# Kernel optimization log

Hardware: AMD Instinct MI355X
Metric: run time of the kernel (lower is better)

## Reference

```python
import jax, jax.numpy as jnp
import numpy as np

B, D, H, W, C = 1, 16, 56, 56, 256
WD, WH, WW = 2, 7, 7
SD, SH, SW = 1, 3, 3
HEADS = 8
HDIM = C // HEADS
N = WD * WH * WW          # 98 tokens per window
NW = (D // WD) * (H // WH) * (W // WW)  # 512 windows per batch element
HID = 4 * C


def _rel_index():
    coords = np.stack(np.meshgrid(np.arange(WD), np.arange(WH), np.arange(WW), indexing='ij')).reshape(3, -1)
    rel = (coords[:, :, None] - coords[:, None, :]).transpose(1, 2, 0).astype(np.int64)
    rel[..., 0] += WD - 1; rel[..., 1] += WH - 1; rel[..., 2] += WW - 1
    rel[..., 0] *= (2 * WH - 1) * (2 * WW - 1)
    rel[..., 1] *= (2 * WW - 1)
    return rel.sum(-1)  # (N, N)

REL_INDEX = jnp.asarray(_rel_index())


def _np_window_partition(x):
    b, d, h, w, c = x.shape
    x = x.reshape(b, d // WD, WD, h // WH, WH, w // WW, WW, c)
    return x.transpose(0, 1, 3, 5, 2, 4, 6, 7).reshape(-1, N, c)


def _compute_mask():
    # Swin compute_mask: label 3x3x3 shifted regions, windows mask cross-region pairs with -100
    img = np.zeros((1, D, H, W, 1), np.float32)
    cnt = 0
    for ds in (slice(0, -WD), slice(-WD, -SD), slice(-SD, None)):
        for hs in (slice(0, -WH), slice(-WH, -SH), slice(-SH, None)):
            for ws in (slice(0, -WW), slice(-WW, -SW), slice(-SW, None)):
                img[:, ds, hs, ws, :] = cnt; cnt += 1
    mw = _np_window_partition(img).reshape(NW, N)
    am = mw[:, None, :] - mw[:, :, None]
    return np.where(am != 0, -100.0, 0.0).astype(np.float32)


def setup_inputs():
    key = jax.random.key(0)
    ks = jax.random.split(key, 8)
    s = 0.02
    return {
        'x': jax.random.normal(ks[0], (B, D, H, W, C), jnp.float32),
        'mask_matrix': jnp.asarray(_compute_mask()),
        'g1': jnp.ones((C,), jnp.float32), 'b1': jnp.zeros((C,), jnp.float32),
        'qkv_w': jax.random.normal(ks[1], (C, 3 * C), jnp.float32) * s,
        'qkv_b': jnp.zeros((3 * C,), jnp.float32),
        'rpb': jax.random.normal(ks[2], ((2 * WD - 1) * (2 * WH - 1) * (2 * WW - 1), HEADS), jnp.float32) * s,
        'proj_w': jax.random.normal(ks[3], (C, C), jnp.float32) * s,
        'proj_b': jnp.zeros((C,), jnp.float32),
        'g2': jnp.ones((C,), jnp.float32), 'b2': jnp.zeros((C,), jnp.float32),
        'fc1_w': jax.random.normal(ks[4], (C, HID), jnp.float32) * s,
        'fc1_b': jnp.zeros((HID,), jnp.float32),
        'fc2_w': jax.random.normal(ks[5], (HID, C), jnp.float32) * s,
        'fc2_b': jnp.zeros((C,), jnp.float32),
    }


def _ln(x, g, b):
    mu = jnp.mean(x, -1, keepdims=True)
    var = jnp.mean((x - mu) ** 2, -1, keepdims=True)
    return (x - mu) * jax.lax.rsqrt(var + 1e-5) * g + b


def _window_partition(x):
    b = x.shape[0]
    x = x.reshape(b, D // WD, WD, H // WH, WH, W // WW, WW, C)
    return x.transpose(0, 1, 3, 5, 2, 4, 6, 7).reshape(-1, N, C)


def _window_reverse(w):
    x = w.reshape(B, D // WD, H // WH, W // WW, WD, WH, WW, C)
    return x.transpose(0, 1, 4, 2, 5, 3, 6, 7).reshape(B, D, H, W, C)


def reference(x, mask_matrix, g1, b1, qkv_w, qkv_b, rpb, proj_w, proj_b, g2, b2, fc1_w, fc1_b, fc2_w, fc2_b):
    shortcut = x
    y = _ln(x, g1, b1)
    # D,H,W divide window sizes -> pad amounts are 0; cyclic shift for SW-MSA
    y = jnp.roll(y, shift=(-SD, -SH, -SW), axis=(1, 2, 3))
    xw = _window_partition(y)                          # (B_, N, C)
    B_ = xw.shape[0]
    qkv = (xw @ qkv_w + qkv_b).reshape(B_, N, 3, HEADS, HDIM)
    q, k, v = jnp.moveaxis(qkv, 2, 0)                  # each (B_, N, HEADS, HDIM)
    q = q * (HDIM ** -0.5)
    attn = jnp.einsum('bnhd,bmhd->bhnm', q, k)         # (B_, HEADS, N, N)
    bias = rpb[REL_INDEX.reshape(-1)].reshape(N, N, HEADS).transpose(2, 0, 1)
    attn = attn + bias[None]
    attn = attn.reshape(B_ // NW, NW, HEADS, N, N) + mask_matrix[None, :, None]
    attn = jax.nn.softmax(attn.reshape(B_, HEADS, N, N), axis=-1)
    out = jnp.einsum('bhnm,bmhd->bnhd', attn, v).reshape(B_, N, C)
    out = out @ proj_w + proj_b
    y = _window_reverse(out)
    y = jnp.roll(y, shift=(SD, SH, SW), axis=(1, 2, 3))
    x = shortcut + y
    h = _ln(x, g2, b2)
    h = jax.nn.gelu(h @ fc1_w + fc1_b, approximate=False)
    h = h @ fc2_w + fc2_b
    return x + h
```

## Files before the change

kernel.cpp:

```cpp
#include <hip/hip_runtime.h>
#include <hip/hip_bf16.h>

typedef __hip_bfloat16 bf16;
typedef __attribute__((ext_vector_type(4))) float f32x4;
typedef __attribute__((ext_vector_type(8))) short bf16x8;

#define MFMA16(a,b,c) __builtin_amdgcn_mfma_f32_16x16x32_bf16((a),(b),(c),0,0,0)

static __device__ inline unsigned short bfbits(float f) {
  __hip_bfloat16 h = __float2bfloat16(f);
  union { __hip_bfloat16 h; unsigned short u; } u;
  u.h = h; return u.u;
}
static __device__ inline float bf2f(unsigned short u) {
  return __uint_as_float(((unsigned int)u) << 16);
}
static __device__ inline void gld16(const void* g, void* l) {
  __builtin_amdgcn_global_load_lds((const __attribute__((address_space(1))) void*)g,
                                   (__attribute__((address_space(3))) void*)l, 16, 0, 0);
}

__global__ __launch_bounds__(256) void transpose_w(const float* __restrict__ src,
                                                   bf16* __restrict__ dst,
                                                   int N, int K, int scaleN, float scale) {
  int idx = blockIdx.x * 256 + threadIdx.x;
  if (idx >= N * K) return;
  int n = idx / K, k = idx - n * K;
  float v = src[(size_t)k * N + n];
  if (n < scaleN) v *= scale;
  dst[idx] = __float2bfloat16(v);
}

__global__ __launch_bounds__(256) void bias_table_bf(const float* __restrict__ rpb,
                                                     unsigned short* __restrict__ biasT) {
  int idx = blockIdx.x * 256 + threadIdx.x;
  if (idx >= 98 * 98) return;
  int nn = idx / 98, mm = idx - nn * 98;
  int ld = nn / 49, lrem = nn - ld * 49, lh = lrem / 7, lw = lrem - lh * 7;
  int md = mm / 49, mrem = mm - md * 49, mh = mrem / 7, mw = mrem - mh * 7;
  int rel = (ld - md + 1) * 169 + (lh - mh + 6) * 13 + (lw - mw + 6);
  #pragma unroll
  for (int h = 0; h < 8; ++h)
    biasT[h * 9604 + mm * 98 + nn] = bfbits(rpb[rel * 8 + h]);
}

__global__ __launch_bounds__(256) void vtrans_k(const unsigned short* __restrict__ v,
                                                unsigned short* __restrict__ vt) {
  __shared__ unsigned short S[98 * 33];
  const unsigned short* src = v + (size_t)blockIdx.x * 3136;
  for (int i = threadIdx.x; i < 3136; i += 256) {
    int n = i >> 5, d = i & 31;
    S[n * 33 + d] = src[i];
  }
  __syncthreads();
  unsigned short* dst = vt + ((size_t)blockIdx.x << 12);
  for (int i = threadIdx.x; i < 4096; i += 256) {
    int d = i >> 7, m = i & 127;
    dst[i] = (m < 98) ? S[m * 33 + d] : (unsigned short)0;
  }
}

__global__ __launch_bounds__(256) void ln_k(const float* __restrict__ x,
                                            const float* __restrict__ g,
                                            const float* __restrict__ bias,
                                            bf16* __restrict__ out, int windowed) {
  const int wid = threadIdx.x >> 6, lane = threadIdx.x & 63;
  const int t = blockIdx.x * 4 + wid;
  int src = t;
  if (windowed) {
    int widx = t / 98, n = t - widx * 98;
    int zd = widx >> 6, zh = (widx >> 3) & 7, zw = widx & 7;
    int ld = n / 49, rem = n - ld * 49, lh = rem / 7, lw = rem - lh * 7;
    int d = zd * 2 + ld, h = zh * 7 + lh, w = zw * 7 + lw;
    int dsrc = (d + 1) & 15;
    int hsrc = h + 3; if (hsrc >= 56) hsrc -= 56;
    int wsrc = w + 3; if (wsrc >= 56) wsrc -= 56;
    src = (dsrc * 56 + hsrc) * 56 + wsrc;
  }
  const float4 v = *(const float4*)(x + (size_t)src * 256 + lane * 4);
  float s1 = v.x + v.y + v.z + v.w;
  float s2 = v.x * v.x + v.y * v.y + v.z * v.z + v.w * v.w;
  #pragma unroll
  for (int d = 1; d < 64; d <<= 1) {
    s1 += __shfl_xor(s1, d);
    s2 += __shfl_xor(s2, d);
  }
  float mu = s1 * (1.f / 256.f);
  float var = s2 * (1.f / 256.f) - mu * mu;
  float rs = rsqrtf(var + 1e-5f);
  const float4 gv = *(const float4*)(g + lane * 4);
  const float4 bv = *(const float4*)(bias + lane * 4);
  ushort4 pk;
  pk.x = bfbits((v.x - mu) * rs * gv.x + bv.x);
  pk.y = bfbits((v.y - mu) * rs * gv.y + bv.y);
  pk.z = bfbits((v.z - mu) * rs * gv.z + bv.z);
  pk.w = bfbits((v.w - mu) * rs * gv.w + bv.w);
  *(ushort4*)((unsigned short*)out + (size_t)t * 256 + lane * 4) = pk;
}

template<int EPI>
__global__ __launch_bounds__(256) void gemm_k(const bf16* __restrict__ A,
                                              const bf16* __restrict__ Bt,
                                              const float* __restrict__ bias,
                                              int N, int K, int NX, int mrow0,
                                              bf16* __restrict__ out_bf,
                                              float* __restrict__ out_f,
                                              const float* __restrict__ add_f) {
  __shared__ bf16 As[2][128 * 32];
  __shared__ bf16 Bs[2][128 * 32];
  const int tid = threadIdx.x;
  const int wid = tid >> 6, lane = tid & 63;
  const int q8 = gridDim.x >> 3;
  const int tile = (blockIdx.x & 7) * q8 + (blockIdx.x >> 3);
  const int bx = tile % NX, by = tile / NX;
  const int row0 = by * 128, col0 = bx * 128;
  const int lrow = tid >> 2, lcol = (tid & 3) * 8;
  const int fr = lane & 15, kh = lane >> 4;
  const int wm = (wid >> 1) * 64, wn = (wid & 1) * 64;
  f32x4 zero4 = {0.f, 0.f, 0.f, 0.f};
  f32x4 acc[4][4];
  #pragma unroll
  for (int i = 0; i < 4; ++i)
    #pragma unroll
    for (int j = 0; j < 4; ++j) acc[i][j] = zero4;

  const bf16* aP = A + (size_t)(row0 + lrow) * K + lcol;
  const bf16* bP = Bt + (size_t)(col0 + lrow) * K + lcol;
  bf16* asD = &As[0][lrow * 32 + lcol];
  bf16* bsD = &Bs[0][lrow * 32 + lcol];

  const int nk = K >> 5;
  gld16(aP, asD);
  gld16(aP + (size_t)64 * K, asD + 2048);
  gld16(bP, bsD);
  gld16(bP + (size_t)64 * K, bsD + 2048);

  int cur = 0;
  for (int t = 0; t < nk; ++t) {
    __syncthreads();
    if (t + 1 < nk) {
      int k0 = (t + 1) * 32;
      bf16* aD = asD + (cur ^ 1) * 4096;
      bf16* bD = bsD + (cur ^ 1) * 4096;
      gld16(aP + k0, aD);
      gld16(aP + (size_t)64 * K + k0, aD + 2048);
      gld16(bP + k0, bD);
      gld16(bP + (size_t)64 * K + k0, bD + 2048);
    }
    const bf16* Ab = As[cur];
    const bf16* Bb = Bs[cur];
    bf16x8 af[4], bfr[4];
    #pragma unroll
    for (int i = 0; i < 4; ++i)
      af[i] = *(const bf16x8*)&Ab[(wm + i * 16 + fr) * 32 + kh * 8];
    #pragma unroll
    for (int j = 0; j < 4; ++j)
      bfr[j] = *(const bf16x8*)&Bb[(wn + j * 16 + fr) * 32 + kh * 8];
    #pragma unroll
    for (int i = 0; i < 4; ++i)
      #pragma unroll
      for (int j = 0; j < 4; ++j)
        acc[i][j] = MFMA16(af[i], bfr[j], acc[i][j]);
    cur ^= 1;
  }

  #pragma unroll
  for (int i = 0; i < 4; ++i) {
    #pragma unroll
    for (int j = 0; j < 4; ++j) {
      #pragma unroll
      for (int r = 0; r < 4; ++r) {
        int row = row0 + wm + i * 16 + kh * 4 + r;
        int col = col0 + wn + j * 16 + fr;
        float bb = bias[col];
        if (EPI == 0 && col < 256) bb *= 0.17677669529663687f;
        float v = acc[i][j][r] + bb;
        if (EPI == 0) {
          int part = col >> 8, head = (col >> 5) & 7, hd = col & 31;
          int widx = row / 98, n = row - widx * 98;
          size_t off = ((size_t)(part * 512 + widx) * 8 + head) * 3136 + (size_t)n * 32 + hd;
          out_bf[off] = __float2bfloat16(v);
        } else if (EPI == 1) {
          int widx = row / 98, n = row - widx * 98;
          int zd = widx >> 6, zh = (widx >> 3) & 7, zw = widx & 7;
          int ld = n / 49, rem = n - ld * 49, lh = rem / 7, lw = rem - lh * 7;
          int d = zd * 2 + ld, h = zh * 7 + lh, w = zw * 7 + lw;
          int dsrc = (d + 1) & 15;
          int hsrc = h + 3; if (hsrc >= 56) hsrc -= 56;
          int wsrc = w + 3; if (wsrc >= 56) wsrc -= 56;
          size_t tok = (size_t)(dsrc * 56 + hsrc) * 56 + wsrc;
          out_f[tok * 256 + col] = add_f[tok * 256 + col] + v;
        } else if (EPI == 2) {
          float gl = 0.5f * v * (1.0f + erff(v * 0.70710678118654752f));
          out_bf[(size_t)row * 1024 + col] = __float2bfloat16(gl);
        } else {
          size_t ro = (size_t)(mrow0 + row);
          out_f[ro * 256 + col] = add_f[ro * 256 + col] + v;
        }
      }
    }
  }
}

__global__ __launch_bounds__(256, 2) void attn_k(const bf16* __restrict__ qkv,
                                                 const unsigned short* __restrict__ vt,
                                                 const unsigned short* __restrict__ bias_bf,
                                                 bf16* __restrict__ out) {
  __shared__ unsigned short Pl[112 * 128];
  __shared__ unsigned short biasS[98 * 100];
  __shared__ unsigned char lblS[112];
  const int tid = threadIdx.x;
  const int widx = blockIdx.x >> 1, hh = blockIdx.x & 1;
  const int wid = tid >> 6, lane = tid & 63;
  const int fr = lane & 15, kh = lane >> 4, kh4 = kh * 4;
  const int tr0 = wid * 2;
  f32x4 zero4 = {0.f, 0.f, 0.f, 0.f};

  if (tid < 112) {
    unsigned char l = 255;
    if (tid < 98) {
      int zd = widx >> 6, zh = (widx >> 3) & 7, zw = widx & 7;
      int ld = tid / 49, rem = tid - ld * 49, lh = rem / 7, lw = rem - lh * 7;
      int d = zd * 2 + ld, h = zh * 7 + lh, w = zw * 7 + lw;
      int cd = (d >= 14) + (d >= 15);
      int ch = (h >= 49) + (h >= 53);
      int cw = (w >= 49) + (w >= 53);
      l = (unsigned char)(cd * 9 + ch * 3 + cw);
    }
    lblS[tid] = l;
  }
  __syncthreads();

  unsigned int lblK[7];
  #pragma unroll
  for (int mt = 0; mt < 7; ++mt)
    lblK[mt] = *(const unsigned int*)&lblS[mt * 16 + kh4];
  const bool t1v = (tr0 + 1) < 7;
  unsigned int lq0 = 0x01010101u * lblS[tr0 * 16 + fr];
  unsigned int lq1 = 0x01010101u * lblS[(t1v ? tr0 + 1 : 0) * 16 + fr];

  for (int it = 0; it < 4; ++it) {
    const int head = hh * 4 + it;
    const unsigned short* qbu = (const unsigned short*)qkv + ((size_t)widx * 8 + head) * 3136;
    const unsigned short* kbu = qbu + (size_t)12845056;
    const unsigned short* brow = bias_bf + head * 9604;
    const unsigned short* vtb = vt + (((size_t)widx * 8 + head) << 12);

    __syncthreads();
    for (int j = tid; j < 4802; j += 256) {
      int n = j / 49, m2 = (j - n * 49) * 2;
      *(unsigned int*)&biasS[n * 100 + m2] = *(const unsigned int*)(brow + n * 98 + m2);
    }

    int qr0 = tr0 * 16 + fr; if (qr0 > 97) qr0 = 97;
    int qr1 = (tr0 + 1) * 16 + fr; if (qr1 > 97) qr1 = 97;
    bf16x8 aq0 = *(const bf16x8*)(qbu + qr0 * 32 + kh * 8);
    bf16x8 aq1 = *(const bf16x8*)(qbu + qr1 * 32 + kh * 8);

    f32x4 s2[2][7];
    #pragma unroll
    for (int a = 0; a < 2; ++a)
      #pragma unroll
      for (int m = 0; m < 7; ++m) s2[a][m] = zero4;
    #pragma unroll
    for (int mt = 0; mt < 7; ++mt) {
      int krow = mt * 16 + fr; if (krow > 97) krow = 97;
      bf16x8 kf = *(const bf16x8*)(kbu + krow * 32 + kh * 8);
      s2[0][mt] = MFMA16(kf, aq0, s2[0][mt]);
      s2[1][mt] = MFMA16(kf, aq1, s2[1][mt]);
    }
    __syncthreads();

    #pragma unroll
    for (int ti = 0; ti < 2; ++ti) {
      int tr = tr0 + ti;
      if (tr < 7) {
        int q = tr * 16 + fr;
        bool rv = q < 98;
        int qc = rv ? q : 0;
        unsigned int lq = (ti == 0) ? lq0 : lq1;
        float mx = -1e30f;
        #pragma unroll
        for (int mt = 0; mt < 7; ++mt) {
          unsigned int df = lblK[mt] ^ lq;
          #pragma unroll
          for (int r = 0; r < 4; ++r) {
            int k = mt * 16 + kh4 + r;
            bool ok = rv && (k < 98);
            float b = bf2f(biasS[(k < 98 ? k : 0) * 100 + qc]);
            float msk = ((df >> (8 * r)) & 255u) ? -100.f : 0.f;
            float sv = ok ? (s2[ti][mt][r] + b + msk) : -1e30f;
            s2[ti][mt][r] = sv;
            mx = fmaxf(mx, sv);
          }
        }
        mx = fmaxf(mx, __shfl_xor(mx, 16));
        mx = fmaxf(mx, __shfl_xor(mx, 32));
        float sum = 0.f;
        #pragma unroll
        for (int mt = 0; mt < 7; ++mt) {
          #pragma unroll
          for (int r = 0; r < 4; ++r) {
            float sv = s2[ti][mt][r];
            float e = (sv > -1e29f) ? __expf(sv - mx) : 0.f;
            s2[ti][mt][r] = e;
            sum += e;
          }
        }
        sum += __shfl_xor(sum, 16);
        sum += __shfl_xor(sum, 32);
        float inv = rv ? (1.0f / sum) : 0.f;
        #pragma unroll
        for (int mt = 0; mt < 7; ++mt) {
          ushort4 pk;
          pk.x = bfbits(s2[ti][mt][0] * inv);
          pk.y = bfbits(s2[ti][mt][1] * inv);
          pk.z = bfbits(s2[ti][mt][2] * inv);
          pk.w = bfbits(s2[ti][mt][3] * inv);
          *(ushort4*)&Pl[(q * 128 + mt * 16 + kh4) ^ ((q & 7) << 3)] = pk;
        }
        ushort4 zz; zz.x = zz.y = zz.z = zz.w = 0;
        *(ushort4*)&Pl[(q * 128 + 112 + kh4) ^ ((q & 7) << 3)] = zz;
      }
    }

    f32x4 o00 = zero4, o01 = zero4, o10 = zero4, o11 = zero4;
    #pragma unroll
    for (int kk = 0; kk < 4; ++kk) {
      bf16x8 vv0 = *(const bf16x8*)(vtb + fr * 128 + kk * 32 + kh * 8);
      bf16x8 vv1 = *(const bf16x8*)(vtb + (16 + fr) * 128 + kk * 32 + kh * 8);
      int prow0 = tr0 * 16 + fr;
      bf16x8 pa0 = *(const bf16x8*)&((const bf16*)Pl)[(prow0 * 128 + kk * 32 + kh * 8) ^ ((prow0 & 7) << 3)];
      o00 = MFMA16(pa0, vv0, o00);
      o01 = MFMA16(pa0, vv1, o01);
      if (t1v) {
        int prow1 = prow0 + 16;
        bf16x8 pa1 = *(const bf16x8*)&((const bf16*)Pl)[(prow1 * 128 + kk * 32 + kh * 8) ^ ((prow1 & 7) << 3)];
        o10 = MFMA16(pa1, vv0, o10);
        o11 = MFMA16(pa1, vv1, o11);
      }
    }
    #pragma unroll
    for (int r = 0; r < 4; ++r) {
      int row = tr0 * 16 + kh4 + r;
      if (row < 98) {
        size_t grow = (size_t)widx * 98 + row;
        out[grow * 256 + head * 32 + fr] = __float2bfloat16(o00[r]);
        out[grow * 256 + head * 32 + 16 + fr] = __float2bfloat16(o01[r]);
      }
    }
    if (t1v) {
      #pragma unroll
      for (int r = 0; r < 4; ++r) {
        int row = (tr0 + 1) * 16 + kh4 + r;
        if (row < 98) {
          size_t grow = (size_t)widx * 98 + row;
          out[grow * 256 + head * 32 + fr] = __float2bfloat16(o10[r]);
          out[grow * 256 + head * 32 + 16 + fr] = __float2bfloat16(o11[r]);
        }
      }
    }
  }
}

extern "C" void kernel_launch(void* const* d_in, const int* in_sizes, int n_in,
                              void* d_out, int out_size, void* d_ws, size_t ws_size,
                              hipStream_t stream) {
  const float* x      = (const float*)d_in[0];
  const float* g1     = (const float*)d_in[2];
  const float* b1     = (const float*)d_in[3];
  const float* qkv_w  = (const float*)d_in[4];
  const float* qkv_b  = (const float*)d_in[5];
  const float* rpb    = (const float*)d_in[6];
  const float* proj_w = (const float*)d_in[7];
  const float* proj_b = (const float*)d_in[8];
  const float* g2     = (const float*)d_in[9];
  const float* b2     = (const float*)d_in[10];
  const float* fc1_w  = (const float*)d_in[11];
  const float* fc1_b  = (const float*)d_in[12];
  const float* fc2_w  = (const float*)d_in[13];
  const float* fc2_b  = (const float*)d_in[14];
  float* outp = (float*)d_out;

  char* ws = (char*)d_ws;
  if (ws_size < (size_t)156237824) return;
  bf16*  wqkvT   = (bf16*)(ws + 0);
  bf16*  wprojT  = (bf16*)(ws + 393216);
  bf16*  wfc1T   = (bf16*)(ws + 524288);
  bf16*  wfc2T   = (bf16*)(ws + 1048576);
  unsigned short* bias_bf = (unsigned short*)(ws + 1572864);
  float* x2      = (float*)(ws + 2097152);
  unsigned short* vtb = (unsigned short*)(ws + 11931648);
  char*  pool    = ws + 53477376;
  bf16*  xw       = (bf16*)pool;
  bf16*  qkvb     = (bf16*)(pool + 25690112);
  bf16*  attn_out = (bf16*)pool;
  bf16*  hbuf     = (bf16*)pool;
  bf16*  hh       = (bf16*)(pool + 25690112);

  transpose_w<<<768, 256, 0, stream>>>(qkv_w, wqkvT, 768, 256, 256, 0.17677669529663687f);
  transpose_w<<<256, 256, 0, stream>>>(proj_w, wprojT, 256, 256, 0, 1.f);
  transpose_w<<<1024, 256, 0, stream>>>(fc1_w, wfc1T, 1024, 256, 0, 1.f);
  transpose_w<<<1024, 256, 0, stream>>>(fc2_w, wfc2T, 256, 1024, 0, 1.f);
  bias_table_bf<<<38, 256, 0, stream>>>(rpb, bias_bf);

  ln_k<<<12544, 256, 0, stream>>>(x, g1, b1, xw, 1);
  gemm_k<0><<<2352, 256, 0, stream>>>(xw, wqkvT, qkv_b, 768, 256, 6, 0, qkvb, nullptr, nullptr);
  vtrans_k<<<4096, 256, 0, stream>>>((const unsigned short*)qkvb + (size_t)2 * 12845056, vtb);
  attn_k<<<1024, 256, 0, stream>>>(qkvb, vtb, bias_bf, attn_out);
  gemm_k<1><<<784, 256, 0, stream>>>(attn_out, wprojT, proj_b, 256, 256, 2, 0, nullptr, x2, x);
  ln_k<<<12544, 256, 0, stream>>>(x2, g2, b2, hbuf, 0);
  for (int ch = 0; ch < 2; ++ch) {
    gemm_k<2><<<1568, 256, 0, stream>>>(hbuf + (size_t)ch * 25088 * 256, wfc1T, fc1_b,
                                        1024, 256, 8, 0, hh, nullptr, nullptr);
    gemm_k<3><<<392, 256, 0, stream>>>(hh, wfc2T, fc2_b, 256, 1024, 2, ch * 25088,
                                       nullptr, outp, x2);
  }
}
```

Before: 326.9 us.

## Deepen GEMM global-to-LDS pipeline to four stages with explicit vmcnt waits

New measurement: 339.3 us. 3.8% more time.

```diff
diff --git a/kernel.cpp b/kernel.cpp
--- a/kernel.cpp
+++ b/kernel.cpp
@@ -106,8 +106,8 @@
                                               bf16* __restrict__ out_bf,
                                               float* __restrict__ out_f,
                                               const float* __restrict__ add_f) {
-  __shared__ bf16 As[2][128 * 32];
-  __shared__ bf16 Bs[2][128 * 32];
+  __shared__ bf16 As[4][128 * 32];
+  __shared__ bf16 Bs[4][128 * 32];
   const int tid = threadIdx.x;
   const int wid = tid >> 6, lane = tid & 63;
   const int q8 = gridDim.x >> 3;
@@ -126,29 +126,18 @@
 
   const bf16* aP = A + (size_t)(row0 + lrow) * K + lcol;
   const bf16* bP = Bt + (size_t)(col0 + lrow) * K + lcol;
-  bf16* asD = &As[0][lrow * 32 + lcol];
-  bf16* bsD = &Bs[0][lrow * 32 + lcol];
-
-  const int nk = K >> 5;
-  gld16(aP, asD);
-  gld16(aP + (size_t)64 * K, asD + 2048);
-  gld16(bP, bsD);
-  gld16(bP + (size_t)64 * K, bsD + 2048);
-
-  int cur = 0;
-  for (int t = 0; t < nk; ++t) {
-    __syncthreads();
-    if (t + 1 < nk) {
-      int k0 = (t + 1) * 32;
-      bf16* aD = asD + (cur ^ 1) * 4096;
-      bf16* bD = bsD + (cur ^ 1) * 4096;
-      gld16(aP + k0, aD);
-      gld16(aP + (size_t)64 * K + k0, aD + 2048);
-      gld16(bP + k0, bD);
-      gld16(bP + (size_t)64 * K + k0, bD + 2048);
-    }
-    const bf16* Ab = As[cur];
-    const bf16* Bb = Bs[cur];
+  const int sOff = lrow * 32 + lcol;
+
+  auto stage = [&](int t) {
+    int k0 = t * 32, s = t & 3;
+    gld16(aP + k0, &As[s][sOff]);
+    gld16(aP + (size_t)64 * K + k0, &As[s][sOff + 2048]);
+    gld16(bP + k0, &Bs[s][sOff]);
+    gld16(bP + (size_t)64 * K + k0, &Bs[s][sOff + 2048]);
+  };
+  auto compute = [&](int s) {
+    const bf16* Ab = As[s];
+    const bf16* Bb = Bs[s];
     bf16x8 af[4], bfr[4];
     #pragma unroll
     for (int i = 0; i < 4; ++i)
@@ -161,8 +150,19 @@
       #pragma unroll
       for (int j = 0; j < 4; ++j)
         acc[i][j] = MFMA16(af[i], bfr[j], acc[i][j]);
-    cur ^= 1;
-  }
+  };
+
+  const int nk = K >> 5;
+  stage(0); stage(1); stage(2);
+  for (int t = 0; t < nk - 2; ++t) {
+    asm volatile("s_waitcnt vmcnt(8)\n\ts_barrier" ::: "memory");
+    if (t + 3 < nk) stage(t + 3);
+    compute(t & 3);
+  }
+  asm volatile("s_waitcnt vmcnt(4)\n\ts_barrier" ::: "memory");
+  compute((nk - 2) & 3);
+  asm volatile("s_waitcnt vmcnt(0)\n\ts_barrier" ::: "memory");
+  compute((nk - 1) & 3);
 
   #pragma unroll
   for (int i = 0; i < 4; ++i) {
```

## Fuse V transpose into QKV GEMM epilogue and read bias from global

Applied to the files above, without the earlier changes.

After: 383.5 us. 1.17x slower.

```diff
diff --git a/kernel.cpp b/kernel.cpp
--- a/kernel.cpp
+++ b/kernel.cpp
@@ -44,19 +44,11 @@
     biasT[h * 9604 + mm * 98 + nn] = bfbits(rpb[rel * 8 + h]);
 }
 
-__global__ __launch_bounds__(256) void vtrans_k(const unsigned short* __restrict__ v,
-                                                unsigned short* __restrict__ vt) {
-  __shared__ unsigned short S[98 * 33];
-  const unsigned short* src = v + (size_t)blockIdx.x * 3136;
-  for (int i = threadIdx.x; i < 3136; i += 256) {
-    int n = i >> 5, d = i & 31;
-    S[n * 33 + d] = src[i];
-  }
-  __syncthreads();
+__global__ __launch_bounds__(256) void vtpad_k(unsigned short* __restrict__ vt) {
   unsigned short* dst = vt + ((size_t)blockIdx.x << 12);
-  for (int i = threadIdx.x; i < 4096; i += 256) {
-    int d = i >> 7, m = i & 127;
-    dst[i] = (m < 98) ? S[m * 33 + d] : (unsigned short)0;
+  for (int i = threadIdx.x; i < 960; i += 256) {
+    int c = i / 30, m = 98 + (i - c * 30);
+    dst[c * 128 + m] = 0;
   }
 }
 
@@ -104,6 +96,7 @@
                                               const float* __restrict__ bias,
                                               int N, int K, int NX, int mrow0,
                                               bf16* __restrict__ out_bf,
+                                              bf16* __restrict__ out_v,
                                               float* __restrict__ out_f,
                                               const float* __restrict__ add_f) {
   __shared__ bf16 As[2][128 * 32];
@@ -178,8 +171,13 @@
         if (EPI == 0) {
           int part = col >> 8, head = (col >> 5) & 7, hd = col & 31;
           int widx = row / 98, n = row - widx * 98;
-          size_t off = ((size_t)(part * 512 + widx) * 8 + head) * 3136 + (size_t)n * 32 + hd;
-          out_bf[off] = __float2bfloat16(v);
+          if (part < 2) {
+            size_t off = ((size_t)(part * 512 + widx) * 8 + head) * 3136 + (size_t)n * 32 + hd;
+            out_bf[off] = __float2bfloat16(v);
+          } else {
+            size_t off = (((size_t)widx * 8 + head) << 12) + (size_t)hd * 128 + n;
+            out_v[off] = __float2bfloat16(v);
+          }
         } else if (EPI == 1) {
           int widx = row / 98, n = row - widx * 98;
           int zd = widx >> 6, zh = (widx >> 3) & 7, zw = widx & 7;
@@ -207,7 +205,6 @@
                                                  const unsigned short* __restrict__ bias_bf,
                                                  bf16* __restrict__ out) {
   __shared__ unsigned short Pl[112 * 128];
-  __shared__ unsigned short biasS[98 * 100];
   __shared__ unsigned char lblS[112];
   const int tid = threadIdx.x;
   const int widx = blockIdx.x >> 1, hh = blockIdx.x & 1;
@@ -246,12 +243,6 @@
     const unsigned short* brow = bias_bf + head * 9604;
     const unsigned short* vtb = vt + (((size_t)widx * 8 + head) << 12);
 
-    __syncthreads();
-    for (int j = tid; j < 4802; j += 256) {
-      int n = j / 49, m2 = (j - n * 49) * 2;
-      *(unsigned int*)&biasS[n * 100 + m2] = *(const unsigned int*)(brow + n * 98 + m2);
-    }
-
     int qr0 = tr0 * 16 + fr; if (qr0 > 97) qr0 = 97;
     int qr1 = (tr0 + 1) * 16 + fr; if (qr1 > 97) qr1 = 97;
     bf16x8 aq0 = *(const bf16x8*)(qbu + qr0 * 32 + kh * 8);
@@ -269,7 +260,6 @@
       s2[0][mt] = MFMA16(kf, aq0, s2[0][mt]);
       s2[1][mt] = MFMA16(kf, aq1, s2[1][mt]);
     }
-    __syncthreads();
 
     #pragma unroll
     for (int ti = 0; ti < 2; ++ti) {
@@ -287,7 +277,7 @@
           for (int r = 0; r < 4; ++r) {
             int k = mt * 16 + kh4 + r;
             bool ok = rv && (k < 98);
-            float b = bf2f(biasS[(k < 98 ? k : 0) * 100 + qc]);
+            float b = bf2f(brow[(k < 98 ? k : 0) * 98 + qc]);
             float msk = ((df >> (8 * r)) & 255u) ? -100.f : 0.f;
             float sv = ok ? (s2[ti][mt][r] + b + msk) : -1e30f;
             s2[ti][mt][r] = sv;
@@ -403,17 +393,19 @@
   transpose_w<<<1024, 256, 0, stream>>>(fc1_w, wfc1T, 1024, 256, 0, 1.f);
   transpose_w<<<1024, 256, 0, stream>>>(fc2_w, wfc2T, 256, 1024, 0, 1.f);
   bias_table_bf<<<38, 256, 0, stream>>>(rpb, bias_bf);
+  vtpad_k<<<4096, 256, 0, stream>>>(vtb);
 
   ln_k<<<12544, 256, 0, stream>>>(x, g1, b1, xw, 1);
-  gemm_k<0><<<2352, 256, 0, stream>>>(xw, wqkvT, qkv_b, 768, 256, 6, 0, qkvb, nullptr, nullptr);
-  vtrans_k<<<4096, 256, 0, stream>>>((const unsigned short*)qkvb + (size_t)2 * 12845056, vtb);
+  gemm_k<0><<<2352, 256, 0, stream>>>(xw, wqkvT, qkv_b, 768, 256, 6, 0,
+                                      qkvb, (bf16*)vtb, nullptr, nullptr);
   attn_k<<<1024, 256, 0, stream>>>(qkvb, vtb, bias_bf, attn_out);
-  gemm_k<1><<<784, 256, 0, stream>>>(attn_out, wprojT, proj_b, 256, 256, 2, 0, nullptr, x2, x);
+  gemm_k<1><<<784, 256, 0, stream>>>(attn_out, wprojT, proj_b, 256, 256, 2, 0,
+                                     nullptr, nullptr, x2, x);
   ln_k<<<12544, 256, 0, stream>>>(x2, g2, b2, hbuf, 0);
   for (int ch = 0; ch < 2; ++ch) {
     gemm_k<2><<<1568, 256, 0, stream>>>(hbuf + (size_t)ch * 25088 * 256, wfc1T, fc1_b,
-                                        1024, 256, 8, 0, hh, nullptr, nullptr);
+                                        1024, 256, 8, 0, hh, nullptr, nullptr, nullptr);
     gemm_k<3><<<392, 256, 0, stream>>>(hh, wfc2T, fc2_b, 256, 1024, 2, ch * 25088,
-                                       nullptr, outp, x2);
-  }
-}
+                                       nullptr, nullptr, outp, x2);
+  }
+}
```
